# Optimization experiments

Measured on AMD Instinct MI355X. Metric: run time of the kernel, lower is better.

## Reference

```python
import jax, jax.numpy as jnp
import numpy as np

B, N_FEAT, D = 16384, 32, 64
HID1, HID2, HOF = 1024, 512, 64
OUT = 1
N_PAIRS = N_FEAT * (N_FEAT - 1) // 2
EPS = 1e-5


def setup_inputs() -> dict:
    key = jax.random.key(0)
    ks = jax.random.split(key, 16)
    s = 0.02
    return {
        "x": jax.random.normal(ks[0], (B, N_FEAT, D), dtype=jnp.float32),
        "W1": jax.random.normal(ks[1], (N_FEAT * D, HID1), dtype=jnp.float32) * s,
        "b1": jnp.zeros((HID1,), jnp.float32),
        "g1": jnp.ones((HID1,), jnp.float32),
        "beta1": jnp.zeros((HID1,), jnp.float32),
        "W2": jax.random.normal(ks[2], (HID1, HID2), dtype=jnp.float32) * s,
        "b2": jnp.zeros((HID2,), jnp.float32),
        "g2": jnp.ones((HID2,), jnp.float32),
        "beta2": jnp.zeros((HID2,), jnp.float32),
        "W3": jax.random.normal(ks[3], (HID2, HOF), dtype=jnp.float32) * s,
        "b3": jnp.zeros((HOF,), jnp.float32),
        "Wc": jax.random.normal(ks[4], (HOF + N_PAIRS, OUT), dtype=jnp.float32) * s,
        "bc": jnp.zeros((OUT,), jnp.float32),
    }


def _batchnorm(h, g, beta):
    # BatchNorm1d in training mode: batch mean / biased variance
    m = jnp.mean(h, axis=0)
    v = jnp.var(h, axis=0)
    return g * (h - m) * jax.lax.rsqrt(v + EPS) + beta


_IU, _JU = np.triu_indices(N_FEAT, k=1)  # same (i<j) order as nested loop


def reference(x, W1, b1, g1, beta1, W2, b2, g2, beta2, W3, b3, Wc, bc):
    # second-order interactions: all pairwise dot products, gathered upper-tri
    gram = jnp.einsum("bnd,bmd->bnm", x, x)          # [B, N, N]
    pairs = gram[:, _IU, _JU]                          # [B, N*(N-1)/2]
    # deep processor
    flat = x.reshape(x.shape[0], -1)                   # [B, N*D]
    h = _batchnorm(jax.nn.relu(flat @ W1 + b1), g1, beta1)
    h = _batchnorm(jax.nn.relu(h @ W2 + b2), g2, beta2)
    hof = h @ W3 + b3                                  # [B, HOF]
    inter = jnp.concatenate([hof, pairs], axis=1)
    return inter @ Wc + bc
```

## Files before the change

kernel.cpp:

```cpp
#include <hip/hip_runtime.h>
#include <stdint.h>

typedef unsigned short u16;
typedef unsigned char u8;
typedef __attribute__((ext_vector_type(8))) short short8;
typedef __attribute__((ext_vector_type(4))) float f32x4;

#define BATCH 16384L
#define WSCALE 64.0f
#define INV_WSCALE (1.0f / 64.0f)

__device__ __forceinline__ u16 f2bf(float f) {
    union { float f; uint32_t u; } cv; cv.f = f;
    uint32_t u = cv.u;
    u = (u + 0x7fffu + ((u >> 16) & 1u)) >> 16;
    return (u16)u;
}
__device__ __forceinline__ float bf2f(u16 h) {
    union { uint32_t u; float f; } cv; cv.u = ((uint32_t)h) << 16;
    return cv.f;
}
template<bool HI>
__device__ __forceinline__ uint32_t fp8pk(float a, float b, uint32_t old) {
    return (uint32_t)__builtin_amdgcn_cvt_pk_fp8_f32(a, b, (int)old, HI);
}
__device__ __forceinline__ u8 f2fp8(float v) {
    return (u8)(__builtin_amdgcn_cvt_pk_fp8_f32(v, v, 0, false) & 0xff);
}

__global__ __launch_bounds__(256) void k_gram(const float* __restrict__ x,
                                              const float* __restrict__ Wc,
                                              u8* __restrict__ xb,
                                              float* __restrict__ spair) {
    const int wave = threadIdx.x >> 6;
    const int lane = threadIdx.x & 63;
    const long b = (long)blockIdx.x * 4 + wave;
    const int r16 = lane & 15, quad = lane >> 4;
    const float* xg = x + b * 2048;

    short8 hi[2][2], lo[2][2];
    for (int mt = 0; mt < 2; mt++) {
        for (int k0 = 0; k0 < 2; k0++) {
            const int row = mt * 16 + r16;
            const int kof = k0 * 32 + quad * 8;
            const float* p = xg + row * 64 + kof;
            float4 p0 = *(const float4*)p;
            float4 p1 = *(const float4*)(p + 4);
            float v[8] = {p0.x, p0.y, p0.z, p0.w, p1.x, p1.y, p1.z, p1.w};
            short8 h, l;
            for (int j = 0; j < 8; j++) {
                u16 hb = f2bf(v[j]);
                h[j] = (short)hb;
                l[j] = (short)f2bf(v[j] - bf2f(hb));
            }
            hi[mt][k0] = h; lo[mt][k0] = l;
            uint32_t w0 = fp8pk<false>(v[0], v[1], 0); w0 = fp8pk<true>(v[2], v[3], w0);
            uint32_t w1 = fp8pk<false>(v[4], v[5], 0); w1 = fp8pk<true>(v[6], v[7], w1);
            *(uint2*)(xb + b * 2048 + row * 64 + kof) = make_uint2(w0, w1);
        }
    }
    f32x4 zero = {0.f, 0.f, 0.f, 0.f};
    f32x4 acc[2][2];
    for (int mt = 0; mt < 2; mt++) for (int nt = 0; nt < 2; nt++) acc[mt][nt] = zero;
    for (int k0 = 0; k0 < 2; k0++)
        for (int mt = 0; mt < 2; mt++)
            for (int nt = 0; nt < 2; nt++) {
                acc[mt][nt] = __builtin_amdgcn_mfma_f32_16x16x32_bf16(hi[mt][k0], hi[nt][k0], acc[mt][nt], 0, 0, 0);
                acc[mt][nt] = __builtin_amdgcn_mfma_f32_16x16x32_bf16(hi[mt][k0], lo[nt][k0], acc[mt][nt], 0, 0, 0);
                acc[mt][nt] = __builtin_amdgcn_mfma_f32_16x16x32_bf16(lo[mt][k0], hi[nt][k0], acc[mt][nt], 0, 0, 0);
            }
    float pacc = 0.f;
    for (int mt = 0; mt < 2; mt++)
        for (int nt = 0; nt < 2; nt++)
            for (int r = 0; r < 4; r++) {
                int row = mt * 16 + quad * 4 + r;
                int col = nt * 16 + r16;
                if (col > row) {
                    int p = 31 * row - (row * (row - 1)) / 2 + (col - row - 1);
                    pacc += acc[mt][nt][r] * Wc[64 + p];
                }
            }
    for (int off = 1; off < 64; off <<= 1) pacc += __shfl_xor(pacc, off);
    if (lane == 0) spair[b] = pacc;
}

__global__ __launch_bounds__(256) void k_transpose_fp8(const float* __restrict__ W,
                                                       const float* __restrict__ scale,
                                                       u8* __restrict__ WT,
                                                       int K, int N) {
    __shared__ float tile[32][33];
    const int nb = blockIdx.x * 32, kb = blockIdx.y * 32;
    const int tx = threadIdx.x & 31, ty = threadIdx.x >> 5;
    if (scale) {
        for (int r = ty; r < 32; r += 8)
            tile[r][tx] = scale[kb + r] * W[(long)(kb + r) * N + nb + tx];
    } else {
        for (int r = ty; r < 32; r += 8)
            tile[r][tx] = W[(long)(kb + r) * N + nb + tx];
    }
    __syncthreads();
    for (int r = ty; r < 32; r += 8)
        WT[(long)(nb + r) * K + kb + tx] = f2fp8(WSCALE * tile[tx][r]);
}

template<int LOGNB>
__global__ __launch_bounds__(256) void gemm_bn(const u8* __restrict__ A,
                                               const u8* __restrict__ Bt,
                                               const float* __restrict__ bias,
                                               u8* __restrict__ C,
                                               float* __restrict__ sums,
                                               float* __restrict__ ssq,
                                               int N, int K, float inv) {
    __shared__ u8 lA[128 * 128];
    __shared__ u8 lB[128 * 128];
    const int tid = threadIdx.x;
    const int lane = tid & 63, wave = tid >> 6;
    const int wm = wave >> 1, wn = wave & 1;
    const int quad = lane >> 4, r16 = lane & 15;
    const int lid = blockIdx.x;
    const int xcd = lid & 7, t = lid >> 3;
    const int nbk = t & ((1 << LOGNB) - 1);
    const int mbk = (xcd << 4) + (t >> LOGNB);
    const long m0 = (long)mbk * 128;
    const long n0 = (long)nbk * 128;

    f32x4 zero = {0.f, 0.f, 0.f, 0.f};
    f32x4 acc[4][4];
    for (int mt = 0; mt < 4; mt++) for (int nt = 0; nt < 4; nt++) acc[mt][nt] = zero;

    const int gcb = quad >> 1, off8 = (quad & 1) * 8;

    for (long k0 = 0; k0 < K; k0 += 128) {
        __syncthreads();
        for (int i = 0; i < 4; i++) {
            const int c = tid + 256 * i;
            const int row = c >> 3, pos = c & 7;
            const int g = pos ^ (row & 7);
            const u8* ga = A + (m0 + row) * K + k0 + g * 16;
            const u8* gb = Bt + (n0 + row) * K + k0 + g * 16;
            __builtin_amdgcn_global_load_lds((const __attribute__((address_space(1))) void*)ga,
                                             (__attribute__((address_space(3))) void*)(&lA[c * 16]), 16, 0, 0);
            __builtin_amdgcn_global_load_lds((const __attribute__((address_space(1))) void*)gb,
                                             (__attribute__((address_space(3))) void*)(&lB[c * 16]), 16, 0, 0);
        }
        __syncthreads();
        for (int ks = 0; ks < 4; ks++) {
            const int gc = ks * 2 + gcb;
            long af[4], bfr[4];
            for (int mt = 0; mt < 4; mt++) {
                const int R = wm * 64 + mt * 16 + r16;
                af[mt] = *(const long*)&lA[R * 128 + ((gc ^ (R & 7)) * 16) + off8];
            }
            for (int nt = 0; nt < 4; nt++) {
                const int R = wn * 64 + nt * 16 + r16;
                bfr[nt] = *(const long*)&lB[R * 128 + ((gc ^ (R & 7)) * 16) + off8];
            }
            for (int mt = 0; mt < 4; mt++)
                for (int nt = 0; nt < 4; nt++)
                    acc[mt][nt] = __builtin_amdgcn_mfma_f32_16x16x32_fp8_fp8(af[mt], bfr[nt], acc[mt][nt], 0, 0, 0);
        }
    }

    for (int nt = 0; nt < 4; nt++) {
        const int col = (int)n0 + wn * 64 + nt * 16 + r16;
        const float bcol = bias[col];
        float s = 0.f, sq = 0.f;
        for (int mt = 0; mt < 4; mt++)
            for (int r = 0; r < 4; r++) {
                const long row = m0 + wm * 64 + mt * 16 + quad * 4 + r;
                float v = acc[mt][nt][r] * inv + bcol;
                v = fmaxf(v, 0.f);
                C[row * N + col] = f2fp8(v);
                s += v; sq += v * v;
            }
        s += __shfl_xor(s, 16);  s += __shfl_xor(s, 32);
        sq += __shfl_xor(sq, 16); sq += __shfl_xor(sq, 32);
        if (quad == 0) { atomicAdd(&sums[col], s); atomicAdd(&ssq[col], sq); }
    }
}

__global__ void k_stat(const float* __restrict__ sums, const float* __restrict__ ssq,
                       const float* __restrict__ g, const float* __restrict__ beta,
                       float* __restrict__ a, float* __restrict__ c, int n, float invB) {
    const int k = blockIdx.x * 256 + threadIdx.x;
    if (k < n) {
        const float m = sums[k] * invB;
        const float var = ssq[k] * invB - m * m;
        const float s = g[k] * rsqrtf(var + 1e-5f);
        a[k] = s; c[k] = beta[k] - s * m;
    }
}

__global__ __launch_bounds__(64) void k_b2adj(const float* __restrict__ W2,
                                              const float* __restrict__ c1,
                                              const float* __restrict__ b2,
                                              float* __restrict__ b2a) {
    const int col = blockIdx.x, lane = threadIdx.x;
    float s = 0.f;
    for (int k = lane; k < 1024; k += 64) s += c1[k] * W2[(long)k * 512 + col];
    for (int off = 1; off < 64; off <<= 1) s += __shfl_xor(s, off);
    if (lane == 0) b2a[col] = b2[col] + s;
}

__global__ void k_v(const float* __restrict__ W3, const float* __restrict__ b3,
                    const float* __restrict__ Wc, const float* __restrict__ bc,
                    float* __restrict__ v, float* __restrict__ c0) {
    const int k = blockIdx.x * 256 + threadIdx.x;
    if (k < 512) {
        float s = 0.f;
        for (int j = 0; j < 64; j++) s += W3[k * 64 + j] * Wc[j];
        v[k] = s;
    }
    if (k == 0) {
        float s = 0.f;
        for (int j = 0; j < 64; j++) s += b3[j] * Wc[j];
        *c0 = s + bc[0];
    }
}

__global__ __launch_bounds__(256) void k_final(const u8* __restrict__ h2,
                                               const float* __restrict__ a2,
                                               const float* __restrict__ c2,
                                               const float* __restrict__ v,
                                               const float* __restrict__ c0,
                                               const float* __restrict__ spair,
                                               float* __restrict__ out) {
    const int wave = threadIdx.x >> 6, lane = threadIdx.x & 63;
    const long b = (long)blockIdx.x * 4 + wave;
    const int k0 = lane * 8;
    uint2 hv = *(const uint2*)&h2[b * 512 + k0];
    float f[8];
    f[0] = __builtin_amdgcn_cvt_f32_fp8(hv.x, 0);
    f[1] = __builtin_amdgcn_cvt_f32_fp8(hv.x, 1);
    f[2] = __builtin_amdgcn_cvt_f32_fp8(hv.x, 2);
    f[3] = __builtin_amdgcn_cvt_f32_fp8(hv.x, 3);
    f[4] = __builtin_amdgcn_cvt_f32_fp8(hv.y, 0);
    f[5] = __builtin_amdgcn_cvt_f32_fp8(hv.y, 1);
    f[6] = __builtin_amdgcn_cvt_f32_fp8(hv.y, 2);
    f[7] = __builtin_amdgcn_cvt_f32_fp8(hv.y, 3);
    float acc = 0.f;
    for (int j = 0; j < 8; j++) {
        const int k = k0 + j;
        acc += (a2[k] * f[j] + c2[k]) * v[k];
    }
    for (int off = 1; off < 64; off <<= 1) acc += __shfl_xor(acc, off);
    if (lane == 0) out[b] = acc + spair[b] + c0[0];
}

extern "C" void kernel_launch(void* const* d_in, const int* in_sizes, int n_in,
                              void* d_out, int out_size, void* d_ws, size_t ws_size,
                              hipStream_t stream) {
    const float* x     = (const float*)d_in[0];
    const float* W1    = (const float*)d_in[1];
    const float* b1    = (const float*)d_in[2];
    const float* g1    = (const float*)d_in[3];
    const float* beta1 = (const float*)d_in[4];
    const float* W2    = (const float*)d_in[5];
    const float* b2    = (const float*)d_in[6];
    const float* g2    = (const float*)d_in[7];
    const float* beta2 = (const float*)d_in[8];
    const float* W3    = (const float*)d_in[9];
    const float* b3    = (const float*)d_in[10];
    const float* Wc    = (const float*)d_in[11];
    const float* bc    = (const float*)d_in[12];
    float* out = (float*)d_out;

    char* ws = (char*)d_ws;
    size_t o = 0;
    u8* xb  = (u8*)(ws + o); o += BATCH * 2048;
    u8* w1f = (u8*)(ws + o); o += 2048L * 1024;
    u8* w2f = (u8*)(ws + o); o += 1024L * 512;
    u8* h1b = (u8*)(ws + o); o += BATCH * 1024;
    u8* h2b = (u8*)(ws + o); o += BATCH * 512;
    float* spair = (float*)(ws + o); o += BATCH * 4;
    float* stats = (float*)(ws + o); o += 3072 * 4;
    float* sums1 = stats, *ssq1 = stats + 1024, *sums2 = stats + 2048, *ssq2 = stats + 2560;
    float* a1 = (float*)(ws + o); o += 1024 * 4;
    float* c1 = (float*)(ws + o); o += 1024 * 4;
    float* a2 = (float*)(ws + o); o += 512 * 4;
    float* c2 = (float*)(ws + o); o += 512 * 4;
    float* vv = (float*)(ws + o); o += 512 * 4;
    float* c0 = (float*)(ws + o); o += 4;
    float* b2a = (float*)(ws + o); o += 512 * 4;

    (void)hipMemsetAsync(stats, 0, 3072 * 4, stream);
    k_gram<<<4096, 256, 0, stream>>>(x, Wc, xb, spair);
    k_transpose_fp8<<<dim3(1024 / 32, 2048 / 32), 256, 0, stream>>>(W1, nullptr, w1f, 2048, 1024);
    gemm_bn<3><<<1024, 256, 0, stream>>>(xb, w1f, b1, h1b, sums1, ssq1, 1024, 2048, INV_WSCALE);
    k_stat<<<4, 256, 0, stream>>>(sums1, ssq1, g1, beta1, a1, c1, 1024, 1.f / 16384.f);
    k_transpose_fp8<<<dim3(512 / 32, 1024 / 32), 256, 0, stream>>>(W2, a1, w2f, 1024, 512);
    k_b2adj<<<512, 64, 0, stream>>>(W2, c1, b2, b2a);
    gemm_bn<2><<<512, 256, 0, stream>>>(h1b, w2f, b2a, h2b, sums2, ssq2, 512, 1024, INV_WSCALE);
    k_stat<<<2, 256, 0, stream>>>(sums2, ssq2, g2, beta2, a2, c2, 512, 1.f / 16384.f);
    k_v<<<2, 256, 0, stream>>>(W3, b3, Wc, bc, vv, c0);
    k_final<<<4096, 256, 0, stream>>>(h2b, a2, c2, vv, c0, spair, out);
}
```

Baseline: 336.6 us.

## Switch FP8 GEMMs to 32x32x64 scaled MFMA and merge small stat kernels

Replaces the 16x16x32 FP8 MFMA inner loop with the gfx950 32x32x64 f8f6f4 scaled MFMA (unit scales), so each wave issues fewer, larger matrix ops and loads 128-bit LDS fragments. The epilogue row mapping and cross-lane reduction are reworked for the 32x32 accumulator layout. Separately, the layer-2 BN stat kernel and the W3·Wc fold kernel are merged into one launch to save launch overhead. The risk lies in the fragment and accumulator layout matching the new instruction; with the same register budget per wave, occupancy may change.

```diff
diff --git a/kernel.cpp b/kernel.cpp
--- a/kernel.cpp
+++ b/kernel.cpp
@@ -5,10 +5,14 @@
 typedef unsigned char u8;
 typedef __attribute__((ext_vector_type(8))) short short8;
 typedef __attribute__((ext_vector_type(4))) float f32x4;
+typedef __attribute__((ext_vector_type(16))) float f32x16;
+typedef __attribute__((ext_vector_type(4))) int i32x4;
+typedef __attribute__((ext_vector_type(8))) int i32x8;
 
 #define BATCH 16384L
 #define WSCALE 64.0f
 #define INV_WSCALE (1.0f / 64.0f)
+#define SCALE_ONE 0x7f7f7f7f
 
 __device__ __forceinline__ u16 f2bf(float f) {
     union { float f; uint32_t u; } cv; cv.f = f;
@@ -103,6 +107,16 @@
         WT[(long)(nb + r) * K + kb + tx] = f2fp8(WSCALE * tile[tx][r]);
 }
 
+__device__ __forceinline__ i32x8 frag32(const u8* __restrict__ lds, int R, int cb) {
+    const int s = R & 7;
+    i32x4 lo = *(const i32x4*)&lds[R * 128 + ((cb ^ s) * 16)];
+    i32x4 hi = *(const i32x4*)&lds[R * 128 + (((cb + 1) ^ s) * 16)];
+    i32x8 r;
+    r[0] = lo[0]; r[1] = lo[1]; r[2] = lo[2]; r[3] = lo[3];
+    r[4] = hi[0]; r[5] = hi[1]; r[6] = hi[2]; r[7] = hi[3];
+    return r;
+}
+
 template<int LOGNB>
 __global__ __launch_bounds__(256) void gemm_bn(const u8* __restrict__ A,
                                                const u8* __restrict__ Bt,
@@ -116,7 +130,7 @@
     const int tid = threadIdx.x;
     const int lane = tid & 63, wave = tid >> 6;
     const int wm = wave >> 1, wn = wave & 1;
-    const int quad = lane >> 4, r16 = lane & 15;
+    const int r32 = lane & 31, hf = lane >> 5;
     const int lid = blockIdx.x;
     const int xcd = lid & 7, t = lid >> 3;
     const int nbk = t & ((1 << LOGNB) - 1);
@@ -124,11 +138,10 @@
     const long m0 = (long)mbk * 128;
     const long n0 = (long)nbk * 128;
 
-    f32x4 zero = {0.f, 0.f, 0.f, 0.f};
-    f32x4 acc[4][4];
-    for (int mt = 0; mt < 4; mt++) for (int nt = 0; nt < 4; nt++) acc[mt][nt] = zero;
-
-    const int gcb = quad >> 1, off8 = (quad & 1) * 8;
+    f32x16 acc[2][2];
+    for (int mt = 0; mt < 2; mt++)
+        for (int nt = 0; nt < 2; nt++)
+            for (int r = 0; r < 16; r++) acc[mt][nt][r] = 0.f;
 
     for (long k0 = 0; k0 < K; k0 += 128) {
         __syncthreads();
@@ -144,38 +157,36 @@
                                              (__attribute__((address_space(3))) void*)(&lB[c * 16]), 16, 0, 0);
         }
         __syncthreads();
-        for (int ks = 0; ks < 4; ks++) {
-            const int gc = ks * 2 + gcb;
-            long af[4], bfr[4];
-            for (int mt = 0; mt < 4; mt++) {
-                const int R = wm * 64 + mt * 16 + r16;
-                af[mt] = *(const long*)&lA[R * 128 + ((gc ^ (R & 7)) * 16) + off8];
-            }
-            for (int nt = 0; nt < 4; nt++) {
-                const int R = wn * 64 + nt * 16 + r16;
-                bfr[nt] = *(const long*)&lB[R * 128 + ((gc ^ (R & 7)) * 16) + off8];
-            }
-            for (int mt = 0; mt < 4; mt++)
-                for (int nt = 0; nt < 4; nt++)
-                    acc[mt][nt] = __builtin_amdgcn_mfma_f32_16x16x32_fp8_fp8(af[mt], bfr[nt], acc[mt][nt], 0, 0, 0);
-        }
-    }
-
-    for (int nt = 0; nt < 4; nt++) {
-        const int col = (int)n0 + wn * 64 + nt * 16 + r16;
+        for (int km = 0; km < 2; km++) {
+            const int cb = km * 4 + hf * 2;
+            i32x8 af[2], bfr[2];
+            for (int mt = 0; mt < 2; mt++)
+                af[mt] = frag32(lA, wm * 64 + mt * 32 + r32, cb);
+            for (int nt = 0; nt < 2; nt++)
+                bfr[nt] = frag32(lB, wn * 64 + nt * 32 + r32, cb);
+            for (int mt = 0; mt < 2; mt++)
+                for (int nt = 0; nt < 2; nt++)
+                    acc[mt][nt] = __builtin_amdgcn_mfma_scale_f32_32x32x64_f8f6f4(
+                        af[mt], bfr[nt], acc[mt][nt], 0, 0,
+                        0, SCALE_ONE, 0, SCALE_ONE);
+        }
+    }
+
+    for (int nt = 0; nt < 2; nt++) {
+        const int col = (int)n0 + wn * 64 + nt * 32 + r32;
         const float bcol = bias[col];
         float s = 0.f, sq = 0.f;
-        for (int mt = 0; mt < 4; mt++)
-            for (int r = 0; r < 4; r++) {
-                const long row = m0 + wm * 64 + mt * 16 + quad * 4 + r;
+        for (int mt = 0; mt < 2; mt++)
+            for (int r = 0; r < 16; r++) {
+                const long row = m0 + wm * 64 + mt * 32 + 4 * hf + (r & 3) + 8 * (r >> 2);
                 float v = acc[mt][nt][r] * inv + bcol;
                 v = fmaxf(v, 0.f);
                 C[row * N + col] = f2fp8(v);
                 s += v; sq += v * v;
             }
-        s += __shfl_xor(s, 16);  s += __shfl_xor(s, 32);
-        sq += __shfl_xor(sq, 16); sq += __shfl_xor(sq, 32);
-        if (quad == 0) { atomicAdd(&sums[col], s); atomicAdd(&ssq[col], sq); }
+        s += __shfl_xor(s, 32);
+        sq += __shfl_xor(sq, 32);
+        if (hf == 0) { atomicAdd(&sums[col], s); atomicAdd(&ssq[col], sq); }
     }
 }
 
@@ -191,6 +202,32 @@
     }
 }
 
+__global__ void k_stat2v(const float* __restrict__ sums, const float* __restrict__ ssq,
+                         const float* __restrict__ g, const float* __restrict__ beta,
+                         float* __restrict__ a, float* __restrict__ c, float invB,
+                         const float* __restrict__ W3, const float* __restrict__ b3,
+                         const float* __restrict__ Wc, const float* __restrict__ bc,
+                         float* __restrict__ v, float* __restrict__ c0) {
+    if (blockIdx.x < 2) {
+        const int k = blockIdx.x * 256 + threadIdx.x;
+        const float m = sums[k] * invB;
+        const float var = ssq[k] * invB - m * m;
+        const float s = g[k] * rsqrtf(var + 1e-5f);
+        a[k] = s; c[k] = beta[k] - s * m;
+    } else {
+        for (int k = threadIdx.x; k < 512; k += 256) {
+            float s = 0.f;
+            for (int j = 0; j < 64; j++) s += W3[k * 64 + j] * Wc[j];
+            v[k] = s;
+        }
+        if (threadIdx.x == 0) {
+            float s = 0.f;
+            for (int j = 0; j < 64; j++) s += b3[j] * Wc[j];
+            *c0 = s + bc[0];
+        }
+    }
+}
+
 __global__ __launch_bounds__(64) void k_b2adj(const float* __restrict__ W2,
                                               const float* __restrict__ c1,
                                               const float* __restrict__ b2,
@@ -200,22 +237,6 @@
     for (int k = lane; k < 1024; k += 64) s += c1[k] * W2[(long)k * 512 + col];
     for (int off = 1; off < 64; off <<= 1) s += __shfl_xor(s, off);
     if (lane == 0) b2a[col] = b2[col] + s;
-}
-
-__global__ void k_v(const float* __restrict__ W3, const float* __restrict__ b3,
-                    const float* __restrict__ Wc, const float* __restrict__ bc,
-                    float* __restrict__ v, float* __restrict__ c0) {
-    const int k = blockIdx.x * 256 + threadIdx.x;
-    if (k < 512) {
-        float s = 0.f;
-        for (int j = 0; j < 64; j++) s += W3[k * 64 + j] * Wc[j];
-        v[k] = s;
-    }
-    if (k == 0) {
-        float s = 0.f;
-        for (int j = 0; j < 64; j++) s += b3[j] * Wc[j];
-        *c0 = s + bc[0];
-    }
 }
 
 __global__ __launch_bounds__(256) void k_final(const u8* __restrict__ h2,
@@ -291,7 +312,7 @@
     k_transpose_fp8<<<dim3(512 / 32, 1024 / 32), 256, 0, stream>>>(W2, a1, w2f, 1024, 512);
     k_b2adj<<<512, 64, 0, stream>>>(W2, c1, b2, b2a);
     gemm_bn<2><<<512, 256, 0, stream>>>(h1b, w2f, b2a, h2b, sums2, ssq2, 512, 1024, INV_WSCALE);
-    k_stat<<<2, 256, 0, stream>>>(sums2, ssq2, g2, beta2, a2, c2, 512, 1.f / 16384.f);
-    k_v<<<2, 256, 0, stream>>>(W3, b3, Wc, bc, vv, c0);
+    k_stat2v<<<3, 256, 0, stream>>>(sums2, ssq2, g2, beta2, a2, c2, 1.f / 16384.f,
+                                    W3, b3, Wc, bc, vv, c0);
     k_final<<<4096, 256, 0, stream>>>(h2b, a2, c2, vv, c0, spair, out);
 }
```

New measurement: 318.1 us. -5.5%, faster.
